# Performance work log

Hardware: AMD Instinct MI355X
Metric: run time of the kernel (lower is better)

The kernel has to match this reference:

```python
import jax, jax.numpy as jnp
import numpy as np

NUM_POPS = 8
K_ACTIVE = 2
IN, OUT = 2048, 2048
BATCH = 8192


def setup_inputs() -> dict:
    key = jax.random.key(0)
    ks = jax.random.split(key, 5)
    scale_in = 1.0 / np.sqrt(IN)
    return {
        "x": jax.random.normal(ks[0], (BATCH, IN), dtype=jnp.float32),
        # expert (population) linear params, stacked: W[p] is [OUT, IN]
        "W": jax.random.uniform(ks[1], (NUM_POPS, OUT, IN), dtype=jnp.float32, minval=-scale_in, maxval=scale_in),
        "b": jax.random.uniform(ks[2], (NUM_POPS, OUT), dtype=jnp.float32, minval=-scale_in, maxval=scale_in),
        # selector linear params
        "Ws": jax.random.uniform(ks[3], (NUM_POPS, IN), dtype=jnp.float32, minval=-scale_in, maxval=scale_in),
        "bs": jax.random.uniform(ks[4], (NUM_POPS,), dtype=jnp.float32, minval=-scale_in, maxval=scale_in),
    }


def reference(x, W, b, Ws, bs):
    # Eval-path math of SimplifiedDRNLayer: per-sample top-k expert selection,
    # uniform mean over the k selected experts' linear outputs.
    logits = x @ Ws.T + bs                      # [B, P]
    probs = jax.nn.softmax(logits, axis=-1)     # [B, P]
    _, topk_idx = jax.lax.top_k(probs, K_ACTIVE)  # [B, k] int32
    # combine weights: 1/k on selected experts, 0 elsewhere
    mask = jax.nn.one_hot(topk_idx, NUM_POPS, dtype=x.dtype).sum(axis=1) / K_ACTIVE  # [B, P]
    # all-expert outputs (P is small/fixed); [B, P, OUT]
    ys = jnp.einsum("poi,bi->bpo", W, x) + b
    out = jnp.einsum("bp,bpo->bo", mask, ys)    # [B, OUT]
    return out
```

## Files before the change

### kernel.cpp

```cpp
#include <hip/hip_runtime.h>
#include <stdint.h>

#define B_ROWS 8192
#define K_DIM 2048
#define N_DIM 2048
#define NPOP 8

typedef float f32x4 __attribute__((ext_vector_type(4)));
typedef __bf16 bf16x8 __attribute__((ext_vector_type(8)));

__device__ __forceinline__ unsigned short f2bf(float f) {
  unsigned int u = __float_as_uint(f);
  u += 0x7fffu + ((u >> 16) & 1u);
  return (unsigned short)(u >> 16);
}

__device__ __forceinline__ void glds16(const unsigned short* g, unsigned short* l) {
  __builtin_amdgcn_global_load_lds(
      (__attribute__((address_space(1))) unsigned int*)g,
      (__attribute__((address_space(3))) unsigned int*)l, 16, 0, 0);
}

__global__ void prep_w_kernel(const float* __restrict__ W, unsigned short* __restrict__ Wb) {
  const int n4 = NPOP * N_DIM * K_DIM / 4;
  int stride = gridDim.x * blockDim.x;
  for (int i = blockIdx.x * blockDim.x + threadIdx.x; i < n4; i += stride) {
    float4 v = reinterpret_cast<const float4*>(W)[i];
    ushort4 s;
    s.x = f2bf(v.x); s.y = f2bf(v.y); s.z = f2bf(v.z); s.w = f2bf(v.w);
    reinterpret_cast<ushort4*>(Wb)[i] = s;
  }
}

__global__ void prep_x_sel_kernel(const float* __restrict__ x,
                                  const float* __restrict__ Ws,
                                  const float* __restrict__ bs,
                                  unsigned short* __restrict__ xb,
                                  int* __restrict__ sel,
                                  float* __restrict__ out) {
  {
    float4 z4 = {0.f, 0.f, 0.f, 0.f};
    float4* o4 = reinterpret_cast<float4*>(out);
    const int n4 = B_ROWS * N_DIM / 4;
    int stride = gridDim.x * blockDim.x;
    for (int i = blockIdx.x * blockDim.x + threadIdx.x; i < n4; i += stride) o4[i] = z4;
  }

  const int w = threadIdx.x >> 6;
  const int l = threadIdx.x & 63;
  const int r = blockIdx.x * 4 + w;

  float acc[NPOP];
#pragma unroll
  for (int p = 0; p < NPOP; ++p) acc[p] = 0.f;

  const float4* x4  = reinterpret_cast<const float4*>(x);
  const float4* Ws4 = reinterpret_cast<const float4*>(Ws);
#pragma unroll
  for (int j = 0; j < 8; ++j) {
    int idx = j * 256 + l * 4;
    float4 v = x4[(r * K_DIM + idx) >> 2];
    ushort4 s; s.x = f2bf(v.x); s.y = f2bf(v.y); s.z = f2bf(v.z); s.w = f2bf(v.w);
    *reinterpret_cast<ushort4*>(xb + (size_t)r * K_DIM + idx) = s;
#pragma unroll
    for (int p = 0; p < NPOP; ++p) {
      float4 wv = Ws4[(p * K_DIM + idx) >> 2];
      acc[p] += v.x * wv.x + v.y * wv.y + v.z * wv.z + v.w * wv.w;
    }
  }
#pragma unroll
  for (int off = 32; off > 0; off >>= 1)
#pragma unroll
    for (int p = 0; p < NPOP; ++p) acc[p] += __shfl_xor(acc[p], off, 64);

  if (l == 0) {
    float lg[NPOP];
#pragma unroll
    for (int p = 0; p < NPOP; ++p) lg[p] = acc[p] + bs[p];
    int p1 = 0;
#pragma unroll
    for (int p = 1; p < NPOP; ++p) if (lg[p] > lg[p1]) p1 = p;
    int p2 = -1;
#pragma unroll
    for (int p = 0; p < NPOP; ++p) {
      if (p == p1) continue;
      if (p2 < 0 || lg[p] > lg[p2]) p2 = p;
    }
    sel[r] = p1 * 8 + p2;
  }
}

__global__ __launch_bounds__(256) void build_lists_kernel(const int* __restrict__ sel,
                                                          int* __restrict__ lists,
                                                          int* __restrict__ cnt) {
  const int lid  = blockIdx.x;
  const int slot = lid >> 3;
  const int ex   = lid & 7;
  const int t    = threadIdx.x;

  __shared__ int psum[256];

  int local[32];
  int c = 0;
#pragma unroll
  for (int i = 0; i < 32; ++i) {
    int r = i * 256 + t;
    int s = sel[r];
    int e = slot ? (s & 7) : (s >> 3);
    if (e == ex) local[c++] = r;
  }
  psum[t] = c;
  __syncthreads();
  for (int off = 1; off < 256; off <<= 1) {
    int v = (t >= off) ? psum[t - off] : 0;
    __syncthreads();
    psum[t] += v;
    __syncthreads();
  }
  int start = psum[t] - c;
  for (int i = 0; i < c; ++i) lists[lid * 2048 + start + i] = local[i];
  if (t == 255) cnt[lid] = psum[255];
}


#define BAR()  asm volatile("s_barrier" ::: "memory")
#define VMW8   asm volatile("s_waitcnt vmcnt(8)" ::: "memory")
#define VMW0   asm volatile("s_waitcnt vmcnt(0)" ::: "memory")
#define SP(x)  __builtin_amdgcn_s_setprio(x)
#define SB0()  __builtin_amdgcn_sched_barrier(0)

#define STAGE_A(buf, msel, kt) do {                                            \
    unsigned short* lb_ = &As[buf][(msel) * 8192 + w * 512];                   \
    glds16((const unsigned short*)((const char*)xb + (aoff##msel##0 + (unsigned)((kt) * 128))), lb_); \
    glds16((const unsigned short*)((const char*)xb + (aoff##msel##1 + (unsigned)((kt) * 128))), lb_ + 4096); \
  } while (0)

#define STAGE_B(buf, nsel, kt) do {                                            \
    unsigned short* lb_ = &Bs[buf][(nsel) * 8192 + w * 512];                   \
    glds16((const unsigned short*)((const char*)wgp + (boff##nsel##0 + (unsigned)((kt) * 128))), lb_); \
    glds16((const unsigned short*)((const char*)wgp + (boff##nsel##1 + (unsigned)((kt) * 128))), lb_ + 4096); \
  } while (0)

#define LOAD_AF(buf, msel) do {                                                \
    const char* ab_ = (const char*)&As[0][0] + (buf) * 32768 + (msel) * 16384 + arow_rd; \
    _Pragma("unroll") for (int mi_ = 0; mi_ < 4; ++mi_) {                      \
      af[mi_][0] = *(const bf16x8*)(ab_ + mi_ * 2048 + csw0);                  \
      af[mi_][1] = *(const bf16x8*)(ab_ + mi_ * 2048 + csw1); }                \
  } while (0)

#define LOAD_BF(dst, buf, nsel) do {                                           \
    const char* bb_ = (const char*)&Bs[0][0] + (buf) * 32768 + (nsel) * 16384 + brow_rd; \
    _Pragma("unroll") for (int ni_ = 0; ni_ < 2; ++ni_) {                      \
      dst[ni_][0] = *(const bf16x8*)(bb_ + ni_ * 2048 + csw0);                 \
      dst[ni_][1] = *(const bf16x8*)(bb_ + ni_ * 2048 + csw1); }               \
  } while (0)

#define MMA(msel, nsel, bfv) do {                                              \
    _Pragma("unroll") for (int mi_ = 0; mi_ < 4; ++mi_)                        \
    _Pragma("unroll") for (int ni_ = 0; ni_ < 2; ++ni_) {                      \
      f32x4 a_ = acc[(msel)*4+mi_][(nsel)*2+ni_];                              \
      a_ = __builtin_amdgcn_mfma_f32_16x16x32_bf16(af[mi_][0], bfv[ni_][0], a_, 0, 0, 0); \
      a_ = __builtin_amdgcn_mfma_f32_16x16x32_bf16(af[mi_][1], bfv[ni_][1], a_, 0, 0, 0); \
      acc[(msel)*4+mi_][(nsel)*2+ni_] = a_; }                                  \
  } while (0)

#define HALF_ITER(buf, kt, DOS, VM) do {                                       \
    LOAD_AF(buf, 0); LOAD_BF(bf0, buf, 0);                                     \
    BAR(); SP(1); MMA(0, 0, bf0); SP(0); SB0(); BAR();                         \
    LOAD_BF(bf1, buf, 1);                                                      \
    if (DOS) STAGE_A(buf, 0, (kt) + 2);                                        \
    BAR(); SP(1); MMA(0, 1, bf1); SP(0); SB0(); BAR();                         \
    LOAD_AF(buf, 1);                                                           \
    if (DOS) { STAGE_B(buf, 0, (kt) + 2); STAGE_B(buf, 1, (kt) + 2); }         \
    BAR(); SP(1); MMA(1, 1, bf1); SP(0); SB0(); BAR();                         \
    if (DOS) STAGE_A(buf, 1, (kt) + 2);                                        \
    VM;                                                                        \
    BAR(); SP(1); MMA(1, 0, bf0); SP(0); SB0(); BAR();                         \
  } while (0)

#define EPILOGUE()                                                             \
  _Pragma("unroll") for (int mi8 = 0; mi8 < 8; ++mi8) {                        \
    const int rb = wm * 128 + ((mi8 >> 2) << 6) + ((mi8 & 3) << 4) + (quad << 2); \
    _Pragma("unroll") for (int j = 0; j < 4; ++j) {                            \
      int r = m0 + rb + j;                                                     \
      if (r < cg) {                                                            \
        int gr = list[r];                                                      \
        float* orow = out + (size_t)gr * N_DIM + n0 + wn * 64;                 \
        _Pragma("unroll") for (int nj = 0; nj < 4; ++nj) {                     \
          int col = ((nj >> 1) << 5) + ((nj & 1) << 4) + lane16;               \
          float v = 0.5f * acc[mi8][nj][j] + 0.5f * bv[nj];                    \
          (void)unsafeAtomicAdd(&orow[col], v);                                \
        } } } }

__global__ __launch_bounds__(512, 2) void gemm_kernel(
    const unsigned short* __restrict__ xb,
    const unsigned short* __restrict__ Wb,
    const float* __restrict__ bvec,
    const int* __restrict__ lists,
    const int* __restrict__ cnt,
    float* __restrict__ out) {
  const int bid  = blockIdx.x;
  const int g    = bid & 7;
  const int mt   = (bid >> 3) & 7;
  const int slot = (bid >> 6) & 1;
  const int nt   = bid >> 7;
  const int lid  = slot * 8 + g;
  const int cg   = cnt[lid];
  const int m0   = mt * 256;
  if (m0 >= cg) return;
  const int n0 = nt * 256;

  __shared__ __align__(16) unsigned short As[2][16384];
  __shared__ __align__(16) unsigned short Bs[2][16384];

  const int t = threadIdx.x;
  const int w = t >> 6, l = t & 63;
  const int lane16 = l & 15, quad = l >> 4;
  const int wm = w >> 2, wn = w & 3;
  const int l8 = l >> 3;
  const unsigned int swS = (unsigned)(((l & 7) ^ l8) << 4);
  const unsigned int swR = (unsigned)((l & 7) << 4);
  const unsigned int csw0 = ((unsigned)(quad << 4)) ^ swR;
  const unsigned int csw1 = ((unsigned)(64 | (quad << 4))) ^ swR;
  const unsigned int arow_rd = (unsigned)(wm * 8192 + lane16 * 128);
  const unsigned int brow_rd = (unsigned)(wn * 4096 + lane16 * 128);

  const int* list = lists + lid * 2048;
  const unsigned short* wgp = Wb + (size_t)g * (N_DIM * K_DIM);

  const int trb = w * 8 + l8;
  int r00 = m0 + trb;        int g00 = (r00 < cg) ? list[r00] : 0;
  int r01 = m0 + 128 + trb;  int g01 = (r01 < cg) ? list[r01] : 0;
  int r10 = m0 + 64 + trb;   int g10 = (r10 < cg) ? list[r10] : 0;
  int r11 = m0 + 192 + trb;  int g11 = (r11 < cg) ? list[r11] : 0;
  const unsigned int aoff00 = (unsigned)g00 * 4096u + swS;
  const unsigned int aoff01 = (unsigned)g01 * 4096u + swS;
  const unsigned int aoff10 = (unsigned)g10 * 4096u + swS;
  const unsigned int aoff11 = (unsigned)g11 * 4096u + swS;
  const int rl0 = w * 8 + l8, rl1 = 64 + w * 8 + l8;
  const int b0 = n0 + ((rl0 >> 5) << 6) + (rl0 & 31);
  const int b1 = n0 + ((rl1 >> 5) << 6) + (rl1 & 31);
  const unsigned int boff00 = (unsigned)b0 * 4096u + swS;
  const unsigned int boff01 = (unsigned)b1 * 4096u + swS;
  const unsigned int boff10 = boff00 + 32u * 4096u;
  const unsigned int boff11 = boff01 + 32u * 4096u;

  bf16x8 af[4][2], bf0[2][2], bf1[2][2];
  f32x4 acc[8][4];
#pragma unroll
  for (int i = 0; i < 8; ++i)
#pragma unroll
    for (int jq = 0; jq < 4; ++jq) { f32x4 z = {0.f, 0.f, 0.f, 0.f}; acc[i][jq] = z; }

  STAGE_A(0, 0, 0); STAGE_B(0, 0, 0); STAGE_B(0, 1, 0); STAGE_A(0, 1, 0);
  STAGE_A(1, 0, 1); STAGE_B(1, 0, 1); STAGE_B(1, 1, 1); STAGE_A(1, 1, 1);
  VMW8;
  BAR();

#pragma unroll 1
  for (int h = 0; h < 30; h += 2) {
    HALF_ITER(0, h,     1, VMW8);
    HALF_ITER(1, h + 1, 1, VMW8);
  }
  HALF_ITER(0, 30, 0, VMW0);
  HALF_ITER(1, 31, 0, (void)0);

  const float* bias = bvec + (size_t)g * N_DIM + n0 + wn * 64;
  float bv[4];
#pragma unroll
  for (int nj = 0; nj < 4; ++nj) bv[nj] = bias[((nj >> 1) << 5) + ((nj & 1) << 4) + lane16];

  EPILOGUE();
}

extern "C" void kernel_launch(void* const* d_in, const int* in_sizes, int n_in,
                              void* d_out, int out_size, void* d_ws, size_t ws_size,
                              hipStream_t stream) {
  const float* x  = (const float*)d_in[0];
  const float* W  = (const float*)d_in[1];
  const float* b  = (const float*)d_in[2];
  const float* Ws = (const float*)d_in[3];
  const float* bs = (const float*)d_in[4];
  float* out = (float*)d_out;

  char* ws = (char*)d_ws;
  unsigned short* Wb = (unsigned short*)ws;
  unsigned short* xb = (unsigned short*)(ws + (size_t)67108864);
  int* lists = (int*)(ws + (size_t)67108864 + 33554432);
  int* cnt   = (int*)(ws + (size_t)67108864 + 33554432 + 131072);
  int* sel   = (int*)(ws + (size_t)67108864 + 33554432 + 131072 + 4096);

  prep_w_kernel<<<4096, 256, 0, stream>>>(W, Wb);
  prep_x_sel_kernel<<<2048, 256, 0, stream>>>(x, Ws, bs, xb, sel, out);
  build_lists_kernel<<<16, 256, 0, stream>>>(sel, lists, cnt);
  gemm_kernel<<<dim3(1024), dim3(512), 0, stream>>>(xb, Wb, b, lists, cnt, out);
}
```

Baseline: 574.3 us.

## Gather selected rows per expert into contiguous bf16 buffer and merge slot lists

```diff
diff --git a/kernel.cpp b/kernel.cpp
--- a/kernel.cpp
+++ b/kernel.cpp
@@ -35,7 +35,6 @@
 __global__ void prep_x_sel_kernel(const float* __restrict__ x,
                                   const float* __restrict__ Ws,
                                   const float* __restrict__ bs,
-                                  unsigned short* __restrict__ xb,
                                   int* __restrict__ sel,
                                   float* __restrict__ out) {
   {
@@ -60,8 +59,6 @@
   for (int j = 0; j < 8; ++j) {
     int idx = j * 256 + l * 4;
     float4 v = x4[(r * K_DIM + idx) >> 2];
-    ushort4 s; s.x = f2bf(v.x); s.y = f2bf(v.y); s.z = f2bf(v.z); s.w = f2bf(v.w);
-    *reinterpret_cast<ushort4*>(xb + (size_t)r * K_DIM + idx) = s;
 #pragma unroll
     for (int p = 0; p < NPOP; ++p) {
       float4 wv = Ws4[(p * K_DIM + idx) >> 2];
@@ -93,10 +90,8 @@
 __global__ __launch_bounds__(256) void build_lists_kernel(const int* __restrict__ sel,
                                                           int* __restrict__ lists,
                                                           int* __restrict__ cnt) {
-  const int lid  = blockIdx.x;
-  const int slot = lid >> 3;
-  const int ex   = lid & 7;
-  const int t    = threadIdx.x;
+  const int ex = blockIdx.x;
+  const int t  = threadIdx.x;
 
   __shared__ int psum[256];
 
@@ -106,8 +101,7 @@
   for (int i = 0; i < 32; ++i) {
     int r = i * 256 + t;
     int s = sel[r];
-    int e = slot ? (s & 7) : (s >> 3);
-    if (e == ex) local[c++] = r;
+    if ((s >> 3) == ex || (s & 7) == ex) local[c++] = r;
   }
   psum[t] = c;
   __syncthreads();
@@ -118,8 +112,47 @@
     __syncthreads();
   }
   int start = psum[t] - c;
-  for (int i = 0; i < c; ++i) lists[lid * 2048 + start + i] = local[i];
-  if (t == 255) cnt[lid] = psum[255];
+  for (int i = 0; i < c; ++i) lists[ex * 8192 + start + i] = local[i];
+  if (t == 255) cnt[ex] = psum[255];
+}
+
+__global__ __launch_bounds__(256) void gather_x_kernel(const float* __restrict__ x,
+                                                       const int* __restrict__ lists,
+                                                       const int* __restrict__ cnt,
+                                                       unsigned short* __restrict__ xg) {
+  const int g  = blockIdx.x;
+  const int mb = blockIdx.y;
+  int cg = 0, base = 0;
+#pragma unroll
+  for (int p = 0; p < NPOP; ++p) {
+    int c = cnt[p];
+    if (p < g) base += (c + 255) & ~255;
+    if (p == g) cg = c;
+  }
+  const int cgpad = (cg + 255) & ~255;
+  const int r0 = mb * 256;
+  if (r0 >= cgpad) return;
+  const int* list = lists + g * 8192;
+  const int t = threadIdx.x;
+
+  for (int i = 0; i < 256; ++i) {
+    int r = r0 + i;
+    uint4* dst = reinterpret_cast<uint4*>(xg + (size_t)(base + r) * K_DIM + t * 8);
+    if (r < cg) {
+      const float* src = x + (size_t)list[r] * K_DIM + t * 8;
+      float4 v0 = *reinterpret_cast<const float4*>(src);
+      float4 v1 = *reinterpret_cast<const float4*>(src + 4);
+      uint4 o;
+      o.x = (unsigned)f2bf(v0.x) | ((unsigned)f2bf(v0.y) << 16);
+      o.y = (unsigned)f2bf(v0.z) | ((unsigned)f2bf(v0.w) << 16);
+      o.z = (unsigned)f2bf(v1.x) | ((unsigned)f2bf(v1.y) << 16);
+      o.w = (unsigned)f2bf(v1.z) | ((unsigned)f2bf(v1.w) << 16);
+      *dst = o;
+    } else {
+      uint4 z = {0u, 0u, 0u, 0u};
+      *dst = z;
+    }
+  }
 }
 
 
@@ -131,14 +164,14 @@
 
 #define STAGE_A(buf, msel, kt) do {                                            \
     unsigned short* lb_ = &As[buf][(msel) * 8192 + w * 512];                   \
-    glds16((const unsigned short*)((const char*)xb + (aoff##msel##0 + (unsigned)((kt) * 128))), lb_); \
-    glds16((const unsigned short*)((const char*)xb + (aoff##msel##1 + (unsigned)((kt) * 128))), lb_ + 4096); \
+    glds16((const unsigned short*)(agp + (aoff##msel##0 + (unsigned)((kt) * 128))), lb_); \
+    glds16((const unsigned short*)(agp + (aoff##msel##1 + (unsigned)((kt) * 128))), lb_ + 4096); \
   } while (0)
 
 #define STAGE_B(buf, nsel, kt) do {                                            \
     unsigned short* lb_ = &Bs[buf][(nsel) * 8192 + w * 512];                   \
-    glds16((const unsigned short*)((const char*)wgp + (boff##nsel##0 + (unsigned)((kt) * 128))), lb_); \
-    glds16((const unsigned short*)((const char*)wgp + (boff##nsel##1 + (unsigned)((kt) * 128))), lb_ + 4096); \
+    glds16((const unsigned short*)(bgp + (boff##nsel##0 + (unsigned)((kt) * 128))), lb_); \
+    glds16((const unsigned short*)(bgp + (boff##nsel##1 + (unsigned)((kt) * 128))), lb_ + 4096); \
   } while (0)
 
 #define LOAD_AF(buf, msel) do {                                                \
@@ -168,10 +201,10 @@
     LOAD_AF(buf, 0); LOAD_BF(bf0, buf, 0);                                     \
     BAR(); SP(1); MMA(0, 0, bf0); SP(0); SB0(); BAR();                         \
     LOAD_BF(bf1, buf, 1);                                                      \
-    if (DOS) STAGE_A(buf, 0, (kt) + 2);                                        \
+    if (DOS) { STAGE_A(buf, 0, (kt) + 2); STAGE_B(buf, 0, (kt) + 2); }         \
     BAR(); SP(1); MMA(0, 1, bf1); SP(0); SB0(); BAR();                         \
     LOAD_AF(buf, 1);                                                           \
-    if (DOS) { STAGE_B(buf, 0, (kt) + 2); STAGE_B(buf, 1, (kt) + 2); }         \
+    if (DOS) STAGE_B(buf, 1, (kt) + 2);                                        \
     BAR(); SP(1); MMA(1, 1, bf1); SP(0); SB0(); BAR();                         \
     if (DOS) STAGE_A(buf, 1, (kt) + 2);                                        \
     VM;                                                                        \
@@ -188,25 +221,29 @@
         float* orow = out + (size_t)gr * N_DIM + n0 + wn * 64;                 \
         _Pragma("unroll") for (int nj = 0; nj < 4; ++nj) {                     \
           int col = ((nj >> 1) << 5) + ((nj & 1) << 4) + lane16;               \
-          float v = 0.5f * acc[mi8][nj][j] + 0.5f * bv[nj];                    \
+          float v = 0.5f * acc[mi8][nj][j] + bv[nj];                           \
           (void)unsafeAtomicAdd(&orow[col], v);                                \
         } } } }
 
 __global__ __launch_bounds__(512, 2) void gemm_kernel(
-    const unsigned short* __restrict__ xb,
+    const unsigned short* __restrict__ xg,
     const unsigned short* __restrict__ Wb,
     const float* __restrict__ bvec,
     const int* __restrict__ lists,
     const int* __restrict__ cnt,
     float* __restrict__ out) {
-  const int bid  = blockIdx.x;
-  const int g    = bid & 7;
-  const int mt   = (bid >> 3) & 7;
-  const int slot = (bid >> 6) & 1;
-  const int nt   = bid >> 7;
-  const int lid  = slot * 8 + g;
-  const int cg   = cnt[lid];
-  const int m0   = mt * 256;
+  const int bid = blockIdx.x;
+  const int g   = bid & 7;
+  const int mt  = (bid >> 3) & 31;
+  const int nt  = bid >> 8;
+  int cg = 0, base = 0;
+#pragma unroll
+  for (int p = 0; p < NPOP; ++p) {
+    int c = cnt[p];
+    if (p < g) base += (c + 255) & ~255;
+    if (p == g) cg = c;
+  }
+  const int m0 = mt * 256;
   if (m0 >= cg) return;
   const int n0 = nt * 256;
 
@@ -225,18 +262,15 @@
   const unsigned int arow_rd = (unsigned)(wm * 8192 + lane16 * 128);
   const unsigned int brow_rd = (unsigned)(wn * 4096 + lane16 * 128);
 
-  const int* list = lists + lid * 2048;
-  const unsigned short* wgp = Wb + (size_t)g * (N_DIM * K_DIM);
+  const int* list = lists + g * 8192;
+  const char* agp = (const char*)(xg + (size_t)(base + m0) * K_DIM);
+  const char* bgp = (const char*)(Wb + (size_t)g * (N_DIM * K_DIM));
 
   const int trb = w * 8 + l8;
-  int r00 = m0 + trb;        int g00 = (r00 < cg) ? list[r00] : 0;
-  int r01 = m0 + 128 + trb;  int g01 = (r01 < cg) ? list[r01] : 0;
-  int r10 = m0 + 64 + trb;   int g10 = (r10 < cg) ? list[r10] : 0;
-  int r11 = m0 + 192 + trb;  int g11 = (r11 < cg) ? list[r11] : 0;
-  const unsigned int aoff00 = (unsigned)g00 * 4096u + swS;
-  const unsigned int aoff01 = (unsigned)g01 * 4096u + swS;
-  const unsigned int aoff10 = (unsigned)g10 * 4096u + swS;
-  const unsigned int aoff11 = (unsigned)g11 * 4096u + swS;
+  const unsigned int aoff00 = (unsigned)((trb)       * 4096) + swS;
+  const unsigned int aoff01 = (unsigned)((128 + trb) * 4096) + swS;
+  const unsigned int aoff10 = (unsigned)((64 + trb)  * 4096) + swS;
+  const unsigned int aoff11 = (unsigned)((192 + trb) * 4096) + swS;
   const int rl0 = w * 8 + l8, rl1 = 64 + w * 8 + l8;
   const int b0 = n0 + ((rl0 >> 5) << 6) + (rl0 & 31);
   const int b1 = n0 + ((rl1 >> 5) << 6) + (rl1 & 31);
@@ -268,7 +302,7 @@
   const float* bias = bvec + (size_t)g * N_DIM + n0 + wn * 64;
   float bv[4];
 #pragma unroll
-  for (int nj = 0; nj < 4; ++nj) bv[nj] = bias[((nj >> 1) << 5) + ((nj & 1) << 4) + lane16];
+  for (int nj = 0; nj < 4; ++nj) bv[nj] = 0.5f * bias[((nj >> 1) << 5) + ((nj & 1) << 4) + lane16];
 
   EPILOGUE();
 }
@@ -285,13 +319,14 @@
 
   char* ws = (char*)d_ws;
   unsigned short* Wb = (unsigned short*)ws;
-  unsigned short* xb = (unsigned short*)(ws + (size_t)67108864);
-  int* lists = (int*)(ws + (size_t)67108864 + 33554432);
-  int* cnt   = (int*)(ws + (size_t)67108864 + 33554432 + 131072);
-  int* sel   = (int*)(ws + (size_t)67108864 + 33554432 + 131072 + 4096);
+  unsigned short* xg = (unsigned short*)(ws + (size_t)67108864);
+  int* lists = (int*)(ws + (size_t)67108864 + 75497472);
+  int* cnt   = (int*)(ws + (size_t)67108864 + 75497472 + 262144);
+  int* sel   = (int*)(ws + (size_t)67108864 + 75497472 + 262144 + 4096);
 
   prep_w_kernel<<<4096, 256, 0, stream>>>(W, Wb);
-  prep_x_sel_kernel<<<2048, 256, 0, stream>>>(x, Ws, bs, xb, sel, out);
-  build_lists_kernel<<<16, 256, 0, stream>>>(sel, lists, cnt);
-  gemm_kernel<<<dim3(1024), dim3(512), 0, stream>>>(xb, Wb, b, lists, cnt, out);
-}
+  prep_x_sel_kernel<<<2048, 256, 0, stream>>>(x, Ws, bs, sel, out);
+  build_lists_kernel<<<8, 256, 0, stream>>>(sel, lists, cnt);
+  gather_x_kernel<<<dim3(8, 32), 256, 0, stream>>>(x, lists, cnt, xg);
+  gemm_kernel<<<dim3(2048), dim3(512), 0, stream>>>(xg, Wb, b, lists, cnt, out);
+}
```

Result: slower. 658.7 us (+14.7%).

## Merge top-k slot lists per expert and shrink GEMM tiles to 128x128

Applied to the files above, without the earlier changes.

```diff
diff --git a/kernel.cpp b/kernel.cpp
--- a/kernel.cpp
+++ b/kernel.cpp
@@ -93,10 +93,8 @@
 __global__ __launch_bounds__(256) void build_lists_kernel(const int* __restrict__ sel,
                                                           int* __restrict__ lists,
                                                           int* __restrict__ cnt) {
-  const int lid  = blockIdx.x;
-  const int slot = lid >> 3;
-  const int ex   = lid & 7;
-  const int t    = threadIdx.x;
+  const int ex = blockIdx.x;
+  const int t  = threadIdx.x;
 
   __shared__ int psum[256];
 
@@ -106,8 +104,7 @@
   for (int i = 0; i < 32; ++i) {
     int r = i * 256 + t;
     int s = sel[r];
-    int e = slot ? (s & 7) : (s >> 3);
-    if (e == ex) local[c++] = r;
+    if ((s >> 3) == ex || (s & 7) == ex) local[c++] = r;
   }
   psum[t] = c;
   __syncthreads();
@@ -118,8 +115,8 @@
     __syncthreads();
   }
   int start = psum[t] - c;
-  for (int i = 0; i < c; ++i) lists[lid * 2048 + start + i] = local[i];
-  if (t == 255) cnt[lid] = psum[255];
+  for (int i = 0; i < c; ++i) lists[ex * 8192 + start + i] = local[i];
+  if (t == 255) cnt[ex] = psum[255];
 }
 
 
@@ -130,48 +127,48 @@
 #define SB0()  __builtin_amdgcn_sched_barrier(0)
 
 #define STAGE_A(buf, msel, kt) do {                                            \
-    unsigned short* lb_ = &As[buf][(msel) * 8192 + w * 512];                   \
+    unsigned short* lb_ = &As[buf][(msel) * 2048 + w * 512];                   \
     glds16((const unsigned short*)((const char*)xb + (aoff##msel##0 + (unsigned)((kt) * 128))), lb_); \
     glds16((const unsigned short*)((const char*)xb + (aoff##msel##1 + (unsigned)((kt) * 128))), lb_ + 4096); \
   } while (0)
 
 #define STAGE_B(buf, nsel, kt) do {                                            \
-    unsigned short* lb_ = &Bs[buf][(nsel) * 8192 + w * 512];                   \
-    glds16((const unsigned short*)((const char*)wgp + (boff##nsel##0 + (unsigned)((kt) * 128))), lb_); \
-    glds16((const unsigned short*)((const char*)wgp + (boff##nsel##1 + (unsigned)((kt) * 128))), lb_ + 4096); \
+    unsigned short* lb_ = &Bs[buf][(nsel) * 2048 + w * 512];                   \
+    glds16((const unsigned short*)(bgp + (boff##nsel##0 + (unsigned)((kt) * 128))), lb_); \
+    glds16((const unsigned short*)(bgp + (boff##nsel##1 + (unsigned)((kt) * 128))), lb_ + 4096); \
   } while (0)
 
 #define LOAD_AF(buf, msel) do {                                                \
-    const char* ab_ = (const char*)&As[0][0] + (buf) * 32768 + (msel) * 16384 + arow_rd; \
-    _Pragma("unroll") for (int mi_ = 0; mi_ < 4; ++mi_) {                      \
+    const char* ab_ = (const char*)&As[0][0] + (buf) * 16384 + (msel) * 4096 + arow_rd; \
+    _Pragma("unroll") for (int mi_ = 0; mi_ < 2; ++mi_) {                      \
       af[mi_][0] = *(const bf16x8*)(ab_ + mi_ * 2048 + csw0);                  \
       af[mi_][1] = *(const bf16x8*)(ab_ + mi_ * 2048 + csw1); }                \
   } while (0)
 
 #define LOAD_BF(dst, buf, nsel) do {                                           \
-    const char* bb_ = (const char*)&Bs[0][0] + (buf) * 32768 + (nsel) * 16384 + brow_rd; \
+    const char* bb_ = (const char*)&Bs[0][0] + (buf) * 16384 + (nsel) * 4096 + brow_rd; \
     _Pragma("unroll") for (int ni_ = 0; ni_ < 2; ++ni_) {                      \
       dst[ni_][0] = *(const bf16x8*)(bb_ + ni_ * 2048 + csw0);                 \
       dst[ni_][1] = *(const bf16x8*)(bb_ + ni_ * 2048 + csw1); }               \
   } while (0)
 
 #define MMA(msel, nsel, bfv) do {                                              \
-    _Pragma("unroll") for (int mi_ = 0; mi_ < 4; ++mi_)                        \
+    _Pragma("unroll") for (int mi_ = 0; mi_ < 2; ++mi_)                        \
     _Pragma("unroll") for (int ni_ = 0; ni_ < 2; ++ni_) {                      \
-      f32x4 a_ = acc[(msel)*4+mi_][(nsel)*2+ni_];                              \
+      f32x4 a_ = acc[(msel)*2+mi_][(nsel)*2+ni_];                              \
       a_ = __builtin_amdgcn_mfma_f32_16x16x32_bf16(af[mi_][0], bfv[ni_][0], a_, 0, 0, 0); \
       a_ = __builtin_amdgcn_mfma_f32_16x16x32_bf16(af[mi_][1], bfv[ni_][1], a_, 0, 0, 0); \
-      acc[(msel)*4+mi_][(nsel)*2+ni_] = a_; }                                  \
+      acc[(msel)*2+mi_][(nsel)*2+ni_] = a_; }                                  \
   } while (0)
 
 #define HALF_ITER(buf, kt, DOS, VM) do {                                       \
     LOAD_AF(buf, 0); LOAD_BF(bf0, buf, 0);                                     \
     BAR(); SP(1); MMA(0, 0, bf0); SP(0); SB0(); BAR();                         \
     LOAD_BF(bf1, buf, 1);                                                      \
-    if (DOS) STAGE_A(buf, 0, (kt) + 2);                                        \
+    if (DOS) { STAGE_A(buf, 0, (kt) + 2); STAGE_B(buf, 0, (kt) + 2); }         \
     BAR(); SP(1); MMA(0, 1, bf1); SP(0); SB0(); BAR();                         \
     LOAD_AF(buf, 1);                                                           \
-    if (DOS) { STAGE_B(buf, 0, (kt) + 2); STAGE_B(buf, 1, (kt) + 2); }         \
+    if (DOS) STAGE_B(buf, 1, (kt) + 2);                                        \
     BAR(); SP(1); MMA(1, 1, bf1); SP(0); SB0(); BAR();                         \
     if (DOS) STAGE_A(buf, 1, (kt) + 2);                                        \
     VM;                                                                        \
@@ -179,76 +176,70 @@
   } while (0)
 
 #define EPILOGUE()                                                             \
-  _Pragma("unroll") for (int mi8 = 0; mi8 < 8; ++mi8) {                        \
-    const int rb = wm * 128 + ((mi8 >> 2) << 6) + ((mi8 & 3) << 4) + (quad << 2); \
+  _Pragma("unroll") for (int a = 0; a < 4; ++a) {                              \
     _Pragma("unroll") for (int j = 0; j < 4; ++j) {                            \
-      int r = m0 + rb + j;                                                     \
+      int r = m0 + wm * 64 + a * 16 + (quad << 2) + j;                         \
       if (r < cg) {                                                            \
         int gr = list[r];                                                      \
         float* orow = out + (size_t)gr * N_DIM + n0 + wn * 64;                 \
-        _Pragma("unroll") for (int nj = 0; nj < 4; ++nj) {                     \
-          int col = ((nj >> 1) << 5) + ((nj & 1) << 4) + lane16;               \
-          float v = 0.5f * acc[mi8][nj][j] + 0.5f * bv[nj];                    \
+        _Pragma("unroll") for (int bq = 0; bq < 4; ++bq) {                     \
+          int col = bq * 16 + lane16;                                          \
+          float v = 0.5f * acc[a][bq][j] + bv[bq];                             \
           (void)unsafeAtomicAdd(&orow[col], v);                                \
         } } } }
 
-__global__ __launch_bounds__(512, 2) void gemm_kernel(
+__global__ __launch_bounds__(256, 2) void gemm_kernel(
     const unsigned short* __restrict__ xb,
     const unsigned short* __restrict__ Wb,
     const float* __restrict__ bvec,
     const int* __restrict__ lists,
     const int* __restrict__ cnt,
     float* __restrict__ out) {
-  const int bid  = blockIdx.x;
-  const int g    = bid & 7;
-  const int mt   = (bid >> 3) & 7;
-  const int slot = (bid >> 6) & 1;
-  const int nt   = bid >> 7;
-  const int lid  = slot * 8 + g;
-  const int cg   = cnt[lid];
-  const int m0   = mt * 256;
+  const int bid = blockIdx.x;
+  const int g   = bid & 7;
+  const int mt  = (bid >> 3) & 63;
+  const int nt  = bid >> 9;
+  const int cg  = cnt[g];
+  const int m0  = mt * 128;
   if (m0 >= cg) return;
-  const int n0 = nt * 256;
-
-  __shared__ __align__(16) unsigned short As[2][16384];
-  __shared__ __align__(16) unsigned short Bs[2][16384];
+  const int n0 = nt * 128;
+
+  __shared__ __align__(16) unsigned short As[2][8192];
+  __shared__ __align__(16) unsigned short Bs[2][8192];
 
   const int t = threadIdx.x;
   const int w = t >> 6, l = t & 63;
   const int lane16 = l & 15, quad = l >> 4;
-  const int wm = w >> 2, wn = w & 3;
+  const int wm = w >> 1, wn = w & 1;
   const int l8 = l >> 3;
   const unsigned int swS = (unsigned)(((l & 7) ^ l8) << 4);
   const unsigned int swR = (unsigned)((l & 7) << 4);
   const unsigned int csw0 = ((unsigned)(quad << 4)) ^ swR;
   const unsigned int csw1 = ((unsigned)(64 | (quad << 4))) ^ swR;
   const unsigned int arow_rd = (unsigned)(wm * 8192 + lane16 * 128);
-  const unsigned int brow_rd = (unsigned)(wn * 4096 + lane16 * 128);
-
-  const int* list = lists + lid * 2048;
-  const unsigned short* wgp = Wb + (size_t)g * (N_DIM * K_DIM);
+  const unsigned int brow_rd = (unsigned)(wn * 8192 + lane16 * 128);
+
+  const int* list = lists + g * 8192;
+  const char* bgp = (const char*)(Wb + (size_t)g * (N_DIM * K_DIM));
 
   const int trb = w * 8 + l8;
-  int r00 = m0 + trb;        int g00 = (r00 < cg) ? list[r00] : 0;
-  int r01 = m0 + 128 + trb;  int g01 = (r01 < cg) ? list[r01] : 0;
-  int r10 = m0 + 64 + trb;   int g10 = (r10 < cg) ? list[r10] : 0;
-  int r11 = m0 + 192 + trb;  int g11 = (r11 < cg) ? list[r11] : 0;
+  int r00 = m0 + trb;       int g00 = (r00 < cg) ? list[r00] : 0;
+  int r01 = m0 + 64 + trb;  int g01 = (r01 < cg) ? list[r01] : 0;
+  int r10 = m0 + 32 + trb;  int g10 = (r10 < cg) ? list[r10] : 0;
+  int r11 = m0 + 96 + trb;  int g11 = (r11 < cg) ? list[r11] : 0;
   const unsigned int aoff00 = (unsigned)g00 * 4096u + swS;
   const unsigned int aoff01 = (unsigned)g01 * 4096u + swS;
   const unsigned int aoff10 = (unsigned)g10 * 4096u + swS;
   const unsigned int aoff11 = (unsigned)g11 * 4096u + swS;
-  const int rl0 = w * 8 + l8, rl1 = 64 + w * 8 + l8;
-  const int b0 = n0 + ((rl0 >> 5) << 6) + (rl0 & 31);
-  const int b1 = n0 + ((rl1 >> 5) << 6) + (rl1 & 31);
-  const unsigned int boff00 = (unsigned)b0 * 4096u + swS;
-  const unsigned int boff01 = (unsigned)b1 * 4096u + swS;
-  const unsigned int boff10 = boff00 + 32u * 4096u;
-  const unsigned int boff11 = boff01 + 32u * 4096u;
-
-  bf16x8 af[4][2], bf0[2][2], bf1[2][2];
-  f32x4 acc[8][4];
-#pragma unroll
-  for (int i = 0; i < 8; ++i)
+  const unsigned int boff00 = (unsigned)(n0 + trb)      * 4096u + swS;
+  const unsigned int boff01 = (unsigned)(n0 + 64 + trb) * 4096u + swS;
+  const unsigned int boff10 = (unsigned)(n0 + 32 + trb) * 4096u + swS;
+  const unsigned int boff11 = (unsigned)(n0 + 96 + trb) * 4096u + swS;
+
+  bf16x8 af[2][2], bf0[2][2], bf1[2][2];
+  f32x4 acc[4][4];
+#pragma unroll
+  for (int i = 0; i < 4; ++i)
 #pragma unroll
     for (int jq = 0; jq < 4; ++jq) { f32x4 z = {0.f, 0.f, 0.f, 0.f}; acc[i][jq] = z; }
 
@@ -268,7 +259,7 @@
   const float* bias = bvec + (size_t)g * N_DIM + n0 + wn * 64;
   float bv[4];
 #pragma unroll
-  for (int nj = 0; nj < 4; ++nj) bv[nj] = bias[((nj >> 1) << 5) + ((nj & 1) << 4) + lane16];
+  for (int bq = 0; bq < 4; ++bq) bv[bq] = 0.5f * bias[bq * 16 + lane16];
 
   EPILOGUE();
 }
@@ -287,11 +278,11 @@
   unsigned short* Wb = (unsigned short*)ws;
   unsigned short* xb = (unsigned short*)(ws + (size_t)67108864);
   int* lists = (int*)(ws + (size_t)67108864 + 33554432);
-  int* cnt   = (int*)(ws + (size_t)67108864 + 33554432 + 131072);
-  int* sel   = (int*)(ws + (size_t)67108864 + 33554432 + 131072 + 4096);
+  int* cnt   = (int*)(ws + (size_t)67108864 + 33554432 + 262144);
+  int* sel   = (int*)(ws + (size_t)67108864 + 33554432 + 262144 + 4096);
 
   prep_w_kernel<<<4096, 256, 0, stream>>>(W, Wb);
   prep_x_sel_kernel<<<2048, 256, 0, stream>>>(x, Ws, bs, xb, sel, out);
-  build_lists_kernel<<<16, 256, 0, stream>>>(sel, lists, cnt);
-  gemm_kernel<<<dim3(1024), dim3(512), 0, stream>>>(xb, Wb, b, lists, cnt, out);
-}
+  build_lists_kernel<<<8, 256, 0, stream>>>(sel, lists, cnt);
+  gemm_kernel<<<dim3(8192), dim3(256), 0, stream>>>(xb, Wb, b, lists, cnt, out);
+}
```

New measurement: 540.7 us. 5.9% less time.
